# Optimization experiments

Hardware: AMD Instinct MI355X
Metric: run time of the kernel (lower is better)

The kernel has to match this reference:

```python
import jax, jax.numpy as jnp
import numpy as np

B, SIZE, L = 64, 2048, 16
A, SED, HID = 64, 64, 256
R, NUM_ACTION = 65536, 16


def setup_inputs() -> dict:
    key = jax.random.key(0)
    ks = jax.random.split(key, 20)
    n = lambda i, shape: jax.random.normal(ks[i], shape, dtype=jnp.float32) * 0.05
    x = jax.random.randint(ks[0], (B, SIZE + L), 0, 2)
    rel_subj = jax.random.randint(ks[1], (R,), 0, SIZE)
    rel_obj = jax.random.randint(ks[2], (R,), 0, SIZE)
    return {
        "x": x,
        "rel_subj": rel_subj,
        "rel_obj": rel_obj,
        "action_emb": n(3, (NUM_ACTION, A)),
        "pos_emb": n(4, (L, A)),
        "state_emb": n(5, (SIZE, SED)),
        "s2r_w1": n(6, (2 * SED, HID)),
        "s2r_b1": n(7, (HID,)),
        "s2r_w2": n(8, (HID, A)),
        "s2r_b2": n(9, (A,)),
        "q_w": n(10, (A, 2 * A)),
        "q_b": n(11, (2 * A,)),
        "ms_w1": n(12, (3 * A, HID)),
        "ms_b1": n(13, (HID,)),
        "ms_w2": n(14, (HID, A)),
        "ms_b2": n(15, (A,)),
        "meta_init": n(16, (A,)),
    }


def reference(x, rel_subj, rel_obj, action_emb, pos_emb, state_emb,
              s2r_w1, s2r_b1, s2r_w2, s2r_b2, q_w, q_b,
              ms_w1, ms_b1, ms_w2, ms_b2, meta_init):
    length = pos_emb.shape[0]
    size = state_emb.shape[0]
    bsz = x.shape[0]
    init = x[:, :size].astype(jnp.float32)          # [B, size]
    actions = x[:, size:]                            # [B, L]
    # sentence = cat(action_embed, position_embed) -> [B, L, 2A]
    sentence = jnp.concatenate(
        [action_emb[actions],
         jnp.broadcast_to(pos_emb[None], (bsz, length, pos_emb.shape[1]))], axis=2)
    # relation_mode == 'deducted': MLP over gathered (subj, obj) state embeddings
    rel_in = jnp.concatenate([state_emb[rel_subj], state_emb[rel_obj]], axis=1)  # [R, 2*SED]
    relation = jax.nn.relu(rel_in @ s2r_w1 + s2r_b1) @ s2r_w2 + s2r_b2           # [R, A]

    def step(carry, _):
        state, meta = carry
        # run_mode == 'attention': attend over sentence, update metaMode
        query = meta @ q_w + q_b                                   # [B, 2A]
        attn = jax.nn.softmax(jnp.einsum('bd,bld->bl', query, sentence), axis=1)
        attended = jnp.einsum('bl,bld->bd', attn, sentence)        # [B, 2A]
        meta = jax.nn.relu(jnp.concatenate([meta, attended], axis=1) @ ms_w1 + ms_b1) @ ms_w2 + ms_b2
        # gated gather-scatter over relation edges
        h = jax.nn.sigmoid(meta @ relation.T)                      # [B, R]
        vals = state[:, rel_subj] * h                              # gather + gate
        nxt = jnp.zeros_like(state).at[:, rel_obj].add(vals)       # scatter-add
        return (nxt, meta), nxt

    meta0 = jnp.broadcast_to(meta_init[None], (bsz, meta_init.shape[0]))
    _, outs = jax.lax.scan(step, (init, meta0), None, length=length)
    return jnp.transpose(outs, (1, 0, 2))  # [B, L, size]
```

## Files before the change

### kernel.cpp

```cpp
#include <hip/hip_runtime.h>

#define B 64
#define SIZE 2048
#define L 16
#define A 64
#define HID 256
#define R_N 65536
#define XCOLS (SIZE + L)
#define ST_ELEMS ((L + 1) * SIZE * B)
#define RPB 128

typedef short bf16x8 __attribute__((ext_vector_type(8)));
typedef float f32x4 __attribute__((ext_vector_type(4)));

__device__ __forceinline__ unsigned short f2bf(float f) {
    unsigned int u = __float_as_uint(f);
    unsigned int r = (u + 0x7fffu + ((u >> 16) & 1u)) >> 16;
    return (unsigned short)r;
}

__global__ __launch_bounds__(256) void k_init(const int* __restrict__ x,
                                              float* __restrict__ ST,
                                              int* __restrict__ hist,
                                              int* __restrict__ cursor) {
    int tid = threadIdx.x;
    float4* z = (float4*)(ST + (size_t)SIZE * B);
    int total4 = L * SIZE * B / 4;
    float4 zv = {0.f, 0.f, 0.f, 0.f};
    for (int i = blockIdx.x * 256 + tid; i < total4; i += gridDim.x * 256)
        z[i] = zv;
    if (blockIdx.x == 32) {
        for (int i = tid; i < 2048; i += 256) {
            hist[i] = 0;
            cursor[i] = 0;
        }
    }
    if (blockIdx.x < 32) {
        __shared__ float tile[64][65];
        int s0 = blockIdx.x * 64;
        for (int i = tid; i < 4096; i += 256) {
            int b = i >> 6, sc = i & 63;
            tile[b][sc] = (float)x[b * XCOLS + s0 + sc];
        }
        __syncthreads();
        for (int i = tid; i < 4096; i += 256) {
            int si = i >> 6, b = i & 63;
            ST[(size_t)(s0 + si) * B + b] = tile[b][si];
        }
    }
}

__global__ __launch_bounds__(256) void k_hist(const int* __restrict__ rel_obj,
                                              int* __restrict__ hist) {
    for (int i = blockIdx.x * 256 + threadIdx.x; i < R_N; i += 64 * 256)
        atomicAdd(&hist[rel_obj[i]], 1);
}

__global__ __launch_bounds__(256) void k_scan(const int* __restrict__ hist,
                                              int* __restrict__ off,
                                              const float* __restrict__ w2,
                                              unsigned short* __restrict__ w2t) {
    int tid = threadIdx.x;
    if (blockIdx.x == 1) {
        for (int i = tid; i < 64 * 256; i += 256) {
            int c = i >> 8, k = i & 255;
            w2t[i] = f2bf(w2[(size_t)k * 64 + c]);
        }
        return;
    }
    __shared__ int tsum[256];
    int v[8], pre[8];
    int s = 0;
#pragma unroll
    for (int i = 0; i < 8; i++) {
        v[i] = hist[tid * 8 + i];
        pre[i] = s;
        s += v[i];
    }
    tsum[tid] = s;
    __syncthreads();
    for (int ofs = 1; ofs < 256; ofs <<= 1) {
        int t = 0;
        if (tid >= ofs) t = tsum[tid - ofs];
        __syncthreads();
        tsum[tid] += t;
        __syncthreads();
    }
    int ebase = tsum[tid] - s;
#pragma unroll
    for (int i = 0; i < 8; i++) off[tid * 8 + i] = ebase + pre[i];
    if (tid == 255) off[2048] = tsum[255];
}

__global__ __launch_bounds__(256) void k_scatter(const int* __restrict__ rel_subj,
                                                 const int* __restrict__ rel_obj,
                                                 const int* __restrict__ off,
                                                 int* __restrict__ cursor,
                                                 int* __restrict__ subjS,
                                                 int* __restrict__ objS) {
    for (int r = blockIdx.x * 256 + threadIdx.x; r < R_N; r += 64 * 256) {
        int obj = rel_obj[r];
        int pos = off[obj] + atomicAdd(&cursor[obj], 1);
        subjS[pos] = rel_subj[r];
        objS[pos] = obj;
    }
}

__global__ __launch_bounds__(256) void k_p12(const float* __restrict__ state_emb,
                                             const float* __restrict__ w1,
                                             float* __restrict__ P1,
                                             float* __restrict__ P2) {
    __shared__ float emb8[8][64];
    int tid = threadIdx.x;
    int sbase = blockIdx.x * 8;
    for (int i = tid; i < 512; i += 256)
        emb8[i >> 6][i & 63] = state_emb[(size_t)(sbase + (i >> 6)) * 64 + (i & 63)];
    __syncthreads();
    float acc1[8], acc2[8];
#pragma unroll
    for (int s = 0; s < 8; s++) { acc1[s] = 0.f; acc2[s] = 0.f; }
    for (int k = 0; k < 64; k++) {
        float wa = w1[(size_t)k * HID + tid];
        float wb = w1[(size_t)(64 + k) * HID + tid];
#pragma unroll
        for (int s = 0; s < 8; s++) {
            acc1[s] += emb8[s][k] * wa;
            acc2[s] += emb8[s][k] * wb;
        }
    }
#pragma unroll
    for (int s = 0; s < 8; s++) {
        P1[(size_t)(sbase + s) * HID + tid] = acc1[s];
        P2[(size_t)(sbase + s) * HID + tid] = acc2[s];
    }
}

__global__ __launch_bounds__(256) void k_rel2(
    const int* __restrict__ subjS, const int* __restrict__ objS,
    const float* __restrict__ P1, const float* __restrict__ P2,
    const float* __restrict__ b1, const unsigned short* __restrict__ w2t,
    const float* __restrict__ b2, unsigned short* __restrict__ relS) {
    __shared__ unsigned short h[128][264];
    int tid = threadIdx.x, lane = tid & 63, w = tid >> 6;
    int rbase = blockIdx.x * 128;
    for (int e = tid; e < 128 * 64; e += 256) {
        int r = e >> 6, jc = (e & 63) * 4;
        int subj = subjS[rbase + r], obj = objS[rbase + r];
        float4 p1 = *(const float4*)&P1[(size_t)subj * HID + jc];
        float4 p2 = *(const float4*)&P2[(size_t)obj * HID + jc];
        float4 bv = *(const float4*)&b1[jc];
        ushort4 hv;
        hv.x = f2bf(fmaxf(p1.x + p2.x + bv.x, 0.f));
        hv.y = f2bf(fmaxf(p1.y + p2.y + bv.y, 0.f));
        hv.z = f2bf(fmaxf(p1.z + p2.z + bv.z, 0.f));
        hv.w = f2bf(fmaxf(p1.w + p2.w + bv.w, 0.f));
        *(ushort4*)&h[r][jc] = hv;
    }
    __syncthreads();
    int lr = lane & 15, lh = lane >> 4;
    f32x4 acc[2][4];
#pragma unroll
    for (int rt = 0; rt < 2; rt++)
#pragma unroll
        for (int ct = 0; ct < 4; ct++) acc[rt][ct] = (f32x4){0.f, 0.f, 0.f, 0.f};
#pragma unroll
    for (int kk = 0; kk < 8; kk++) {
        bf16x8 bfr[4], afr[2];
#pragma unroll
        for (int ct = 0; ct < 4; ct++)
            bfr[ct] = *(const bf16x8*)(w2t + (ct * 16 + lr) * 256 + kk * 32 + lh * 8);
#pragma unroll
        for (int rt = 0; rt < 2; rt++)
            afr[rt] = *(const bf16x8*)&h[w * 32 + rt * 16 + lr][kk * 32 + lh * 8];
#pragma unroll
        for (int rt = 0; rt < 2; rt++)
#pragma unroll
            for (int ct = 0; ct < 4; ct++)
                acc[rt][ct] = __builtin_amdgcn_mfma_f32_16x16x32_bf16(
                    afr[rt], bfr[ct], acc[rt][ct], 0, 0, 0);
    }
    float b2v[4];
#pragma unroll
    for (int ct = 0; ct < 4; ct++) b2v[ct] = b2[ct * 16 + lr];
#pragma unroll
    for (int rt = 0; rt < 2; rt++)
#pragma unroll
        for (int ct = 0; ct < 4; ct++)
#pragma unroll
            for (int rg = 0; rg < 4; rg++) {
                int row = rbase + w * 32 + rt * 16 + lh * 4 + rg;
                relS[(size_t)row * 64 + ct * 16 + lr] =
                    f2bf(acc[rt][ct][rg] + b2v[ct]);
            }
}

__global__ __launch_bounds__(1024) void k_meta(
    const int* __restrict__ x, const float* __restrict__ action_emb,
    const float* __restrict__ pos_emb, const float* __restrict__ q_w,
    const float* __restrict__ q_b, const float* __restrict__ ms_w1,
    const float* __restrict__ ms_b1, const float* __restrict__ ms_w2,
    const float* __restrict__ ms_b2, const float* __restrict__ meta_init,
    unsigned short* __restrict__ metas_bf) {
    __shared__ float sent[L][132];
    __shared__ float qs[A][17];
    __shared__ float qb_lds[L];
    __shared__ float meta_lds[A];
    __shared__ float logits_lds[L];
    __shared__ float attn_lds[L];
    __shared__ float hidden_lds[HID];
    __shared__ float parts[16][65];
    __shared__ float b2_lds[A];
    int tid = threadIdx.x;
    int b = blockIdx.x;
    int lane = tid & 63, wv = tid >> 6;

    for (int i = tid; i < L * 128; i += 1024) {
        int l = i >> 7, d = i & 127;
        float v;
        if (d < 64)
            v = action_emb[x[b * XCOLS + SIZE + l] * 64 + d];
        else
            v = pos_emb[l * 64 + (d - 64)];
        sent[l][d] = v;
    }
    if (tid < A) {
        meta_lds[tid] = meta_init[tid];
        b2_lds[tid] = ms_b2[tid];
    }
    __syncthreads();

    {
        int k = tid >> 4, l = tid & 15;
        float a = 0.f;
        for (int j = 0; j < 128; j++) a += q_w[(size_t)k * 128 + j] * sent[l][j];
        qs[k][l] = a;
    }
    if (tid < L) {
        float a = 0.f;
        for (int j = 0; j < 128; j++) a += q_b[j] * sent[tid][j];
        qb_lds[tid] = a;
    }
    int j_h = tid >> 2, q_h = tid & 3;
    float w1a_r[16];
#pragma unroll
    for (int i = 0; i < 16; i++)
        w1a_r[i] = ms_w1[(size_t)(q_h * 16 + i) * HID + j_h];
    float sentw_r[4];
#pragma unroll
    for (int i = 0; i < 4; i++) sentw_r[i] = 0.f;
    for (int d = 0; d < 128; d++) {
        float w = ms_w1[(size_t)(64 + d) * HID + j_h];
#pragma unroll
        for (int i = 0; i < 4; i++) sentw_r[i] += sent[q_h * 4 + i][d] * w;
    }
    float b1_r = ms_b1[j_h];
    int g_m = tid >> 6, c_m = tid & 63;
    float w2_r[16];
#pragma unroll
    for (int i = 0; i < 16; i++)
        w2_r[i] = ms_w2[(size_t)(g_m * 16 + i) * 64 + c_m];
    __syncthreads();

    for (int t = 0; t < L; t++) {
        float p = meta_lds[lane] * qs[lane][wv];
        p += __shfl_xor(p, 32);
        p += __shfl_xor(p, 16);
        p += __shfl_xor(p, 8);
        p += __shfl_xor(p, 4);
        p += __shfl_xor(p, 2);
        p += __shfl_xor(p, 1);
        if (lane == 0) logits_lds[wv] = p + qb_lds[wv];
        __syncthreads();
        if (tid < L) {
            float mx = logits_lds[0];
#pragma unroll
            for (int l = 1; l < L; l++) mx = fmaxf(mx, logits_lds[l]);
            float sum = 0.f;
#pragma unroll
            for (int l = 0; l < L; l++) sum += __expf(logits_lds[l] - mx);
            attn_lds[tid] = __expf(logits_lds[tid] - mx) / sum;
        }
        __syncthreads();
        float h = 0.f;
#pragma unroll
        for (int i = 0; i < 16; i++) h += meta_lds[q_h * 16 + i] * w1a_r[i];
#pragma unroll
        for (int i = 0; i < 4; i++) h += attn_lds[q_h * 4 + i] * sentw_r[i];
        h += __shfl_xor(h, 1);
        h += __shfl_xor(h, 2);
        if (q_h == 0) hidden_lds[j_h] = fmaxf(h + b1_r, 0.f);
        __syncthreads();
        float pp = 0.f;
#pragma unroll
        for (int i = 0; i < 16; i++) pp += hidden_lds[g_m * 16 + i] * w2_r[i];
        parts[g_m][c_m] = pp;
        __syncthreads();
        if (tid < A) {
            float nm = b2_lds[tid];
#pragma unroll
            for (int g = 0; g < 16; g++) nm += parts[g][tid];
            meta_lds[tid] = nm;
            metas_bf[((size_t)t * B + b) * A + tid] = f2bf(nm);
        }
        __syncthreads();
    }
}

__global__ __launch_bounds__(256) void k_step(
    const int* __restrict__ off, const int* __restrict__ subjS,
    const int* __restrict__ objS, const unsigned short* __restrict__ relS,
    const unsigned short* __restrict__ mb, const float* __restrict__ st_in,
    float* __restrict__ st_out) {
    __shared__ float vals[RPB][66];
    int tid = threadIdx.x, lane = tid & 63, w = tid >> 6;
    int rbase = blockIdx.x * RPB;
    int base_w = rbase + w * 32;
    int lr = lane & 15, lh = lane >> 4;

    float sv[32];
    int ob[32];
#pragma unroll
    for (int rr = 0; rr < 32; rr++) {
        sv[rr] = st_in[(size_t)subjS[base_w + rr] * B + lane];
        ob[rr] = objS[base_w + rr];
    }

    bf16x8 bfrag[4][2];
#pragma unroll
    for (int ct = 0; ct < 4; ct++)
#pragma unroll
        for (int kk = 0; kk < 2; kk++)
            bfrag[ct][kk] =
                *(const bf16x8*)(mb + (ct * 16 + lr) * 64 + kk * 32 + lh * 8);
    bf16x8 afrag[2][2];
#pragma unroll
    for (int rt = 0; rt < 2; rt++)
#pragma unroll
        for (int kk = 0; kk < 2; kk++)
            afrag[rt][kk] = *(const bf16x8*)(relS +
                (size_t)(rbase + w * 32 + rt * 16 + lr) * 64 + kk * 32 + lh * 8);

    f32x4 acc[2][4];
#pragma unroll
    for (int rt = 0; rt < 2; rt++)
#pragma unroll
        for (int ct = 0; ct < 4; ct++) {
            f32x4 c = {0.f, 0.f, 0.f, 0.f};
            c = __builtin_amdgcn_mfma_f32_16x16x32_bf16(afrag[rt][0],
                                                        bfrag[ct][0], c, 0, 0, 0);
            c = __builtin_amdgcn_mfma_f32_16x16x32_bf16(afrag[rt][1],
                                                        bfrag[ct][1], c, 0, 0, 0);
            acc[rt][ct] = c;
        }
#pragma unroll
    for (int rt = 0; rt < 2; rt++)
#pragma unroll
        for (int ct = 0; ct < 4; ct++)
#pragma unroll
            for (int rg = 0; rg < 4; rg++) {
                int r_loc = w * 32 + rt * 16 + lh * 4 + rg;
                int c = ct * 16 + lr;
                vals[r_loc][c] = 1.f / (1.f + __expf(-acc[rt][ct][rg]));
            }
    __syncthreads();

    float acc_s = 0.f;
    int cur = ob[0];
#pragma unroll
    for (int rr = 0; rr < 32; rr++) {
        float v = vals[w * 32 + rr][lane] * sv[rr];
        if (ob[rr] != cur) {
            int s = off[cur], e = off[cur + 1];
            if (s >= base_w && e <= base_w + 32)
                st_out[(size_t)cur * B + lane] = acc_s;
            else
                atomicAdd(&st_out[(size_t)cur * B + lane], acc_s);
            acc_s = 0.f;
            cur = ob[rr];
        }
        acc_s += v;
    }
    {
        int s = off[cur], e = off[cur + 1];
        if (s >= base_w && e <= base_w + 32)
            st_out[(size_t)cur * B + lane] = acc_s;
        else
            atomicAdd(&st_out[(size_t)cur * B + lane], acc_s);
    }
}

__global__ __launch_bounds__(256) void k_out(const float* __restrict__ ST,
                                             float* __restrict__ out) {
    __shared__ float tile[64][65];
    int t = blockIdx.x >> 5;
    int s0 = (blockIdx.x & 31) * 64;
    const float* src = ST + (size_t)(t + 1) * SIZE * B;
    int tid = threadIdx.x;
    for (int i = tid; i < 64 * 64; i += 256) {
        int si = i >> 6, b = i & 63;
        tile[si][b] = src[(size_t)(s0 + si) * B + b];
    }
    __syncthreads();
    for (int i = tid; i < 64 * 64; i += 256) {
        int b = i >> 6, si = i & 63;
        out[((size_t)b * L + t) * SIZE + s0 + si] = tile[si][b];
    }
}

extern "C" void kernel_launch(void* const* d_in, const int* in_sizes, int n_in,
                              void* d_out, int out_size, void* d_ws,
                              size_t ws_size, hipStream_t stream) {
    const int* x = (const int*)d_in[0];
    const int* rel_subj = (const int*)d_in[1];
    const int* rel_obj = (const int*)d_in[2];
    const float* action_emb = (const float*)d_in[3];
    const float* pos_emb = (const float*)d_in[4];
    const float* state_emb = (const float*)d_in[5];
    const float* s2r_w1 = (const float*)d_in[6];
    const float* s2r_b1 = (const float*)d_in[7];
    const float* s2r_w2 = (const float*)d_in[8];
    const float* s2r_b2 = (const float*)d_in[9];
    const float* q_w = (const float*)d_in[10];
    const float* q_b = (const float*)d_in[11];
    const float* ms_w1 = (const float*)d_in[12];
    const float* ms_b1 = (const float*)d_in[13];
    const float* ms_w2 = (const float*)d_in[14];
    const float* ms_b2 = (const float*)d_in[15];
    const float* meta_init = (const float*)d_in[16];

    float* ws = (float*)d_ws;
    float* ST = ws;
    unsigned short* relS = (unsigned short*)(ws + ST_ELEMS);
    unsigned short* metas_bf = relS + (size_t)R_N * 64;
    float* P1 = (float*)(metas_bf + (size_t)L * B * A);
    float* P2 = P1 + SIZE * HID;
    int* ibase = (int*)(P2 + SIZE * HID);
    int* hist = ibase;
    int* off = ibase + 2048;
    int* cursor = off + 2049;
    int* subjS = cursor + 2048;
    int* objS = subjS + R_N;
    unsigned short* w2t = (unsigned short*)d_out;
    float* out = (float*)d_out;

    k_init<<<256, 256, 0, stream>>>(x, ST, hist, cursor);
    k_hist<<<64, 256, 0, stream>>>(rel_obj, hist);
    k_scan<<<2, 256, 0, stream>>>(hist, off, s2r_w2, w2t);
    k_scatter<<<64, 256, 0, stream>>>(rel_subj, rel_obj, off, cursor, subjS, objS);
    k_p12<<<SIZE / 8, 256, 0, stream>>>(state_emb, s2r_w1, P1, P2);
    k_rel2<<<R_N / RPB, 256, 0, stream>>>(subjS, objS, P1, P2, s2r_b1, w2t,
                                          s2r_b2, relS);
    k_meta<<<B, 1024, 0, stream>>>(x, action_emb, pos_emb, q_w, q_b, ms_w1,
                                   ms_b1, ms_w2, ms_b2, meta_init, metas_bf);
    for (int t = 0; t < L; t++) {
        k_step<<<R_N / RPB, 256, 0, stream>>>(
            off, subjS, objS, relS, metas_bf + (size_t)t * B * A,
            ST + (size_t)t * SIZE * B, ST + (size_t)(t + 1) * SIZE * B);
    }
    k_out<<<512, 256, 0, stream>>>(ST, out);
}
```

Before: 339.3 us.

## Fuse all scan steps and output transpose into one cooperative persistent kernel

Replaces the 16 per-step k_step launches and the k_out launch with a single cooperative kernel of 256 blocks that loops over time steps and uses grid.sync between them. Subject gather offsets and per-run segment masks are computed once and kept in registers across all steps, and the output transpose runs inside the same kernel. This aims to remove launch overhead and repeated index loads. In exchange it adds grid-wide barrier cost, halves the grid (256 rows per block), and raises register pressure from the 64-entry offset array. If the cooperative launch fails, the code falls back to the old multi-launch path.

Result: slower. 801.8 us (+136.3%).

```diff
diff --git a/kernel.cpp b/kernel.cpp
--- a/kernel.cpp
+++ b/kernel.cpp
@@ -1,4 +1,7 @@
 #include <hip/hip_runtime.h>
+#include <hip/hip_cooperative_groups.h>
+
+namespace cg = cooperative_groups;
 
 #define B 64
 #define SIZE 2048
@@ -9,6 +12,7 @@
 #define XCOLS (SIZE + L)
 #define ST_ELEMS ((L + 1) * SIZE * B)
 #define RPB 128
+#define RPC 256
 
 typedef short bf16x8 __attribute__((ext_vector_type(8)));
 typedef float f32x4 __attribute__((ext_vector_type(4)));
@@ -306,6 +310,142 @@
     }
 }
 
+__global__ __launch_bounds__(256, 2) void k_steps(
+    const int* __restrict__ off, const int* __restrict__ subjS,
+    const int* __restrict__ objS, const unsigned short* __restrict__ relS,
+    const unsigned short* __restrict__ metas_bf, float* __restrict__ ST,
+    float* __restrict__ out) {
+    cg::grid_group grid = cg::this_grid();
+    __shared__ float vals[4][32][66];
+    __shared__ int obj_l[RPC];
+    int tid = threadIdx.x, lane = tid & 63, w = tid >> 6;
+    int rbase = blockIdx.x * RPC;
+    int lr = lane & 15, lh = lane >> 4;
+
+    for (int i = tid; i < RPC; i += 256) obj_l[i] = objS[rbase + i];
+    __syncthreads();
+
+    unsigned mnew0 = 0, mcont0 = 0, mnew1 = 0, mcont1 = 0;
+#pragma unroll
+    for (int win = 0; win < 2; win++) {
+        unsigned mn = 0, mc = 0;
+        int lbase = w * 64 + win * 32;
+        int gb = rbase + lbase;
+        int obprev = -1;
+#pragma unroll
+        for (int rr = 0; rr < 32; rr++) {
+            int o = obj_l[lbase + rr];
+            if (o != obprev) {
+                mn |= 1u << rr;
+                if (off[o] >= gb && off[o + 1] <= gb + 32) mc |= 1u << rr;
+            }
+            obprev = o;
+        }
+        if (win == 0) { mnew0 = mn; mcont0 = mc; }
+        else { mnew1 = mn; mcont1 = mc; }
+    }
+    int goff[64];
+#pragma unroll
+    for (int rr = 0; rr < 64; rr++)
+        goff[rr] = subjS[rbase + w * 64 + rr] * B + lane;
+
+    for (int t = 0; t < L; t++) {
+        const unsigned short* mb = metas_bf + (size_t)t * B * A;
+        const float* st_in = ST + (size_t)t * SIZE * B;
+        float* st_out = ST + (size_t)(t + 1) * SIZE * B;
+
+        bf16x8 bfrag[4][2];
+#pragma unroll
+        for (int ct = 0; ct < 4; ct++)
+#pragma unroll
+            for (int kk = 0; kk < 2; kk++)
+                bfrag[ct][kk] =
+                    *(const bf16x8*)(mb + (ct * 16 + lr) * 64 + kk * 32 + lh * 8);
+
+#pragma unroll
+        for (int win = 0; win < 2; win++) {
+            int lbase = w * 64 + win * 32;
+            int gb = rbase + lbase;
+            unsigned mnew = win ? mnew1 : mnew0;
+            unsigned mcont = win ? mcont1 : mcont0;
+
+            float sv[32];
+#pragma unroll
+            for (int rr = 0; rr < 32; rr++) sv[rr] = st_in[goff[win * 32 + rr]];
+
+            bf16x8 afrag[2][2];
+#pragma unroll
+            for (int rt = 0; rt < 2; rt++)
+#pragma unroll
+                for (int kk = 0; kk < 2; kk++)
+                    afrag[rt][kk] = *(const bf16x8*)(relS +
+                        (size_t)(gb + rt * 16 + lr) * 64 + kk * 32 + lh * 8);
+
+            f32x4 acc[2][4];
+#pragma unroll
+            for (int rt = 0; rt < 2; rt++)
+#pragma unroll
+                for (int ct = 0; ct < 4; ct++) {
+                    f32x4 c = {0.f, 0.f, 0.f, 0.f};
+                    c = __builtin_amdgcn_mfma_f32_16x16x32_bf16(
+                        afrag[rt][0], bfrag[ct][0], c, 0, 0, 0);
+                    c = __builtin_amdgcn_mfma_f32_16x16x32_bf16(
+                        afrag[rt][1], bfrag[ct][1], c, 0, 0, 0);
+                    acc[rt][ct] = c;
+                }
+#pragma unroll
+            for (int rt = 0; rt < 2; rt++)
+#pragma unroll
+                for (int ct = 0; ct < 4; ct++)
+#pragma unroll
+                    for (int rg = 0; rg < 4; rg++)
+                        vals[w][rt * 16 + lh * 4 + rg][ct * 16 + lr] =
+                            1.f / (1.f + __expf(-acc[rt][ct][rg]));
+
+            float acc_s = 0.f;
+            int curr = 0;
+#pragma unroll
+            for (int rr = 0; rr < 32; rr++) {
+                if (rr > 0 && ((mnew >> rr) & 1u)) {
+                    int o = obj_l[lbase + curr];
+                    if ((mcont >> curr) & 1u)
+                        st_out[(size_t)o * B + lane] = acc_s;
+                    else
+                        atomicAdd(&st_out[(size_t)o * B + lane], acc_s);
+                    acc_s = 0.f;
+                    curr = rr;
+                }
+                acc_s += vals[w][rr][lane] * sv[rr];
+            }
+            {
+                int o = obj_l[lbase + curr];
+                if ((mcont >> curr) & 1u)
+                    st_out[(size_t)o * B + lane] = acc_s;
+                else
+                    atomicAdd(&st_out[(size_t)o * B + lane], acc_s);
+            }
+        }
+        grid.sync();
+    }
+
+    float(*tile)[65] = (float(*)[65])vals;
+    for (int task = blockIdx.x; task < 512; task += 256) {
+        int t = task >> 5;
+        int s0 = (task & 31) * 64;
+        const float* src = ST + (size_t)(t + 1) * SIZE * B;
+        __syncthreads();
+        for (int i = tid; i < 64 * 64; i += 256) {
+            int si = i >> 6, b = i & 63;
+            tile[si][b] = src[(size_t)(s0 + si) * B + b];
+        }
+        __syncthreads();
+        for (int i = tid; i < 64 * 64; i += 256) {
+            int b = i >> 6, si = i & 63;
+            out[((size_t)b * L + t) * SIZE + s0 + si] = tile[si][b];
+        }
+    }
+}
+
 __global__ __launch_bounds__(256) void k_step(
     const int* __restrict__ off, const int* __restrict__ subjS,
     const int* __restrict__ objS, const unsigned short* __restrict__ relS,
@@ -452,10 +592,19 @@
                                           s2r_b2, relS);
     k_meta<<<B, 1024, 0, stream>>>(x, action_emb, pos_emb, q_w, q_b, ms_w1,
                                    ms_b1, ms_w2, ms_b2, meta_init, metas_bf);
-    for (int t = 0; t < L; t++) {
-        k_step<<<R_N / RPB, 256, 0, stream>>>(
-            off, subjS, objS, relS, metas_bf + (size_t)t * B * A,
-            ST + (size_t)t * SIZE * B, ST + (size_t)(t + 1) * SIZE * B);
-    }
-    k_out<<<512, 256, 0, stream>>>(ST, out);
-}
+
+    void* args[] = {(void*)&off,   (void*)&subjS,    (void*)&objS,
+                    (void*)&relS,  (void*)&metas_bf, (void*)&ST,
+                    (void*)&out};
+    hipError_t ce = hipLaunchCooperativeKernel((const void*)k_steps,
+                                               dim3(R_N / RPC), dim3(256), args,
+                                               0, stream);
+    if (ce != hipSuccess) {
+        for (int t = 0; t < L; t++) {
+            k_step<<<R_N / RPB, 256, 0, stream>>>(
+                off, subjS, objS, relS, metas_bf + (size_t)t * B * A,
+                ST + (size_t)t * SIZE * B, ST + (size_t)(t + 1) * SIZE * B);
+        }
+        k_out<<<512, 256, 0, stream>>>(ST, out);
+    }
+}
```
